# Kernel optimization log

Measured on AMD Instinct MI355X. Metric: run time of the kernel, lower is better.

## Reference

```python
import jax, jax.numpy as jnp
import numpy as np

V = 12288      # HEALPix vertices (nside=32)
C_IN = 128
C_OUT = 128
K = 4          # Chebyshev polynomial degree
DEG = 9        # nnz per Laplacian row (8 neighbors + self)
B = 8
BN_EPS = 1e-5


def setup_inputs() -> dict:
    key = jax.random.key(0)
    kx, kc, kv, kw = jax.random.split(key, 4)
    x = jax.random.normal(kx, (B, V, C_IN), dtype=jnp.float32)
    # sparse Laplacian as COO edge list: 9 entries per row
    lap_rows = jnp.repeat(jnp.arange(V, dtype=jnp.int32), DEG)          # [E]
    lap_cols = jax.random.randint(kc, (V * DEG,), 0, V, dtype=jnp.int32)
    lap_vals = jax.random.normal(kv, (V * DEG,), dtype=jnp.float32) * 0.1
    # Chebyshev weight [Fin*K, Fout] (Fin-major, K-minor, matching [B,V,Fin,K] reshape)
    weight = jax.random.normal(kw, (C_IN * K, C_OUT), dtype=jnp.float32) * (1.0 / np.sqrt(C_IN * K))
    gamma = jnp.ones((C_OUT,), dtype=jnp.float32)
    beta = jnp.zeros((C_OUT,), dtype=jnp.float32)
    return {"x": x, "lap_rows": lap_rows, "lap_cols": lap_cols,
            "lap_vals": lap_vals, "weight": weight, "gamma": gamma, "beta": beta}


def reference(x, lap_rows, lap_cols, lap_vals, weight, gamma, beta):
    b, v, c = x.shape
    k = weight.shape[0] // c

    def spmm(y):
        # y: [B, V, C] -> L @ y along vertex dim
        y2 = y.transpose(1, 0, 2).reshape(v, b * c)                 # [V, B*C]
        g = lap_vals[:, None] * y2[lap_cols]                        # [E, B*C]
        out = jnp.zeros((v, b * c), dtype=y.dtype).at[lap_rows].add(g)
        return out.reshape(v, b, c).transpose(1, 0, 2)              # [B, V, C]

    # Chebyshev recursion: T0 = x, T1 = L x, Tk = 2 L T_{k-1} - T_{k-2}
    terms = [x]
    if k > 1:
        terms.append(spmm(x))
    for _ in range(2, k):
        terms.append(2.0 * spmm(terms[-1]) - terms[-2])
    xk = jnp.stack(terms, axis=-1)                                  # [B, V, C, K]
    conv = jnp.einsum('bvck,cko->bvo', xk.reshape(b, v, c, k),
                      weight.reshape(c, k, -1))                     # [B, V, Cout]

    # BatchNorm1d over [B, Cout, V]: stats over (batch, vertices) per channel
    h = conv.transpose(0, 2, 1)                                     # [B, Cout, V]
    mean = jnp.mean(h, axis=(0, 2), keepdims=True)
    var = jnp.var(h, axis=(0, 2), keepdims=True)
    hn = (h - mean) * jax.lax.rsqrt(var + BN_EPS)
    return hn * gamma[None, :, None] + beta[None, :, None]          # [B, Cout, V]
```

## Files before the change

### kernel.cpp

```cpp
#include <hip/hip_runtime.h>

#define NV    12288
#define CIN   128
#define COUT  128
#define DEG   9
#define NB    8
#define NROWS (NB * NV)
#define KTOT  512
#define BM    384

typedef unsigned short bfu;
typedef __attribute__((ext_vector_type(8))) short short8;
typedef __attribute__((ext_vector_type(4))) float floatx4;
typedef __attribute__((ext_vector_type(4))) unsigned short ushort4v;

__device__ __forceinline__ float bf2f(unsigned short u) {
    union { unsigned int i; float f; } x;
    x.i = ((unsigned int)u) << 16;
    return x.f;
}
__device__ __forceinline__ unsigned short f2bf(float f) {
    union { float f; unsigned int i; } x;
    x.f = f;
    unsigned int r = x.i + 0x7FFFu + ((x.i >> 16) & 1u);
    return (unsigned short)(r >> 16);
}
__device__ __forceinline__ void gload16(const void* g, void* l) {
    __builtin_amdgcn_global_load_lds(
        (const __attribute__((address_space(1))) unsigned int*)g,
        (__attribute__((address_space(3))) unsigned int*)l, 16, 0, 0);
}

__global__ __launch_bounds__(256)
void prep_kernel(const float* __restrict__ x, bfu* __restrict__ xb,
                 const float* __restrict__ W, bfu* __restrict__ Wt,
                 float* __restrict__ stats)
{
    const int blk = blockIdx.x;
    const int t   = threadIdx.x;
    if (blk < 6144) {
        const size_t i = ((size_t)blk * 256 + t) * 8;
        const float4 a = *reinterpret_cast<const float4*>(x + i);
        const float4 b = *reinterpret_cast<const float4*>(x + i + 4);
        short8 r;
        r[0] = (short)f2bf(a.x); r[1] = (short)f2bf(a.y);
        r[2] = (short)f2bf(a.z); r[3] = (short)f2bf(a.w);
        r[4] = (short)f2bf(b.x); r[5] = (short)f2bf(b.y);
        r[6] = (short)f2bf(b.z); r[7] = (short)f2bf(b.w);
        *reinterpret_cast<short8*>(xb + i) = r;
    } else if (blk < 6400) {
        const int i = (blk - 6144) * 256 + t;
        const int o = i >> 9;
        const int kap = i & 511;
        const int s = kap >> 7;
        const int c = kap & 127;
        Wt[i] = f2bf(W[(size_t)(c * 4 + s) * COUT + o]);
    } else {
        stats[t] = 0.f;
    }
}

__global__ __launch_bounds__(256)
void spmm_bf16(const bfu* __restrict__ src, const bfu* __restrict__ sub,
               bfu* __restrict__ outp, const int* __restrict__ cols,
               const float* __restrict__ vals)
{
    const int t  = threadIdx.x;
    const int b  = blockIdx.x & 7;
    const int vt = blockIdx.x >> 3;
    const int v  = vt * 16 + (t >> 4);
    const int c0 = (t & 15) * 8;

    int   ec[DEG];
    float ev[DEG];
#pragma unroll
    for (int e = 0; e < DEG; ++e) {
        ec[e] = cols[v * DEG + e];
        ev[e] = vals[v * DEG + e];
    }

    float acc[8];
#pragma unroll
    for (int j = 0; j < 8; ++j) acc[j] = 0.f;

    const size_t bbase = (size_t)b * NV * CIN;
#pragma unroll
    for (int e = 0; e < DEG; ++e) {
        const short8 s = *reinterpret_cast<const short8*>(
            src + bbase + (size_t)ec[e] * CIN + c0);
#pragma unroll
        for (int j = 0; j < 8; ++j)
            acc[j] = fmaf(ev[e], bf2f((unsigned short)s[j]), acc[j]);
    }

    if (sub != nullptr) {
        const short8 s0 = *reinterpret_cast<const short8*>(
            sub + bbase + (size_t)v * CIN + c0);
#pragma unroll
        for (int j = 0; j < 8; ++j)
            acc[j] = 2.f * acc[j] - bf2f((unsigned short)s0[j]);
    }

    short8 r;
#pragma unroll
    for (int j = 0; j < 8; ++j) r[j] = (short)f2bf(acc[j]);
    *reinterpret_cast<short8*>(outp + bbase + (size_t)v * CIN + c0) = r;
}

__global__ __launch_bounds__(512)
void gemm_mfma(const bfu* __restrict__ A0, const bfu* __restrict__ A1,
               const bfu* __restrict__ A2, const bfu* __restrict__ A3,
               const bfu* __restrict__ Wt, bfu* __restrict__ convT,
               float* __restrict__ gstats)
{
    extern __shared__ char smem[];

    const int t    = threadIdx.x;
    const int lane = t & 63;
    const int wid  = t >> 6;
    const int wr   = wid >> 1;
    const int wc   = wid & 1;
    const int rbase = blockIdx.x * BM;

    floatx4 acc[6][4];
#pragma unroll
    for (int m = 0; m < 6; ++m)
#pragma unroll
        for (int n = 0; n < 4; ++n) acc[m][n] = (floatx4){0.f, 0.f, 0.f, 0.f};

    const bfu* segs[4] = {A0, A1, A2, A3};

#define STAGE(KT, BUF)                                                        \
    {                                                                         \
        const bfu* As_ = segs[(KT) >> 2];                                     \
        const int  cb_ = ((KT) & 3) * 32;                                     \
        _Pragma("unroll")                                                     \
        for (int p = 0; p < 3; ++p) {                                         \
            const int flat = p * 512 + t;                                     \
            const int rr   = flat >> 2;                                       \
            const int ck   = flat & 3;                                        \
            gload16(As_ + (size_t)(rbase + rr) * CIN + cb_                    \
                        + ((ck ^ ((rr >> 1) & 3)) << 3),                      \
                    smem + (BUF) * 24576 + flat * 16);                        \
        }                                                                     \
        {                                                                     \
            const int nn = t >> 2;                                            \
            const int ck = t & 3;                                             \
            gload16(Wt + (size_t)nn * KTOT + (KT) * 32                        \
                       + ((ck ^ ((nn >> 1) & 3)) << 3),                       \
                    smem + 73728 + (BUF) * 8192 + t * 16);                    \
        }                                                                     \
    }

    STAGE(0, 0);
    STAGE(1, 1);
    asm volatile("s_waitcnt vmcnt(4)\n\ts_barrier" ::: "memory");

    const int rsw   = ((lane & 15) >> 1) & 3;
    const int chunk = ((lane >> 4) ^ rsw) * 16;

#pragma unroll
    for (int kt = 0; kt < 16; ++kt) {
        if (kt + 2 < 16) STAGE(kt + 2, (kt + 2) % 3);

        const char* abase = smem + (kt % 3) * 24576;
        const char* bbase = smem + 73728 + (kt % 3) * 8192;
        short8 a[6], b[4];
#pragma unroll
        for (int m = 0; m < 6; ++m)
            a[m] = *reinterpret_cast<const short8*>(
                abase + (wr * 96 + m * 16 + (lane & 15)) * 64 + chunk);
#pragma unroll
        for (int n = 0; n < 4; ++n)
            b[n] = *reinterpret_cast<const short8*>(
                bbase + (wc * 64 + n * 16 + (lane & 15)) * 64 + chunk);
#pragma unroll
        for (int m = 0; m < 6; ++m)
#pragma unroll
            for (int n = 0; n < 4; ++n)
                acc[m][n] = __builtin_amdgcn_mfma_f32_16x16x32_bf16(
                    a[m], b[n], acc[m][n], 0, 0, 0);

        if (kt <= 13)
            asm volatile("s_waitcnt vmcnt(4)\n\ts_barrier" ::: "memory");
        else if (kt == 14)
            asm volatile("s_waitcnt vmcnt(0)\n\ts_barrier" ::: "memory");
    }
#undef STAGE

    __syncthreads();
    float* sred = (float*)smem;
    float* qred = sred + COUT;
    if (t < COUT) { sred[t] = 0.f; qred[t] = 0.f; }
    __syncthreads();

    const int batch = rbase / NV;
    const int v0 = (rbase % NV) + wr * 96 + (lane >> 4) * 4;
    const int ob = wc * 64 + (lane & 15);

#pragma unroll
    for (int n = 0; n < 4; ++n) {
        const int o = ob + n * 16;
        float s = 0.f, q = 0.f;
        bfu* cbase = convT + ((size_t)batch * COUT + o) * NV + v0;
#pragma unroll
        for (int m = 0; m < 6; ++m) {
            const floatx4 v4 = acc[m][n];
            ushort4v r;
#pragma unroll
            for (int j = 0; j < 4; ++j) {
                r[j] = f2bf(v4[j]);
                s += v4[j];
                q = fmaf(v4[j], v4[j], q);
            }
            *reinterpret_cast<ushort4v*>(cbase + m * 16) = r;
        }
        s += __shfl_xor(s, 16); s += __shfl_xor(s, 32);
        q += __shfl_xor(q, 16); q += __shfl_xor(q, 32);
        if ((lane >> 4) == 0) {
            atomicAdd(&sred[o], s);
            atomicAdd(&qred[o], q);
        }
    }
    __syncthreads();
    if (t < COUT) {
        atomicAdd(&gstats[t], sred[t]);
        atomicAdd(&gstats[COUT + t], qred[t]);
    }
}

__global__ __launch_bounds__(256)
void normalize_bn(const bfu* __restrict__ convT, const float* __restrict__ stats,
                  const float* __restrict__ gamma, const float* __restrict__ beta,
                  float* __restrict__ outp)
{
    const size_t i = ((size_t)blockIdx.x * 256 + threadIdx.x) * 8;
    const int ch = (int)((i / NV) & (COUT - 1));
    const float invN = 1.0f / (float)NROWS;
    const float mean = stats[ch] * invN;
    const float var  = stats[COUT + ch] * invN - mean * mean;
    const float rsig = rsqrtf(var + 1e-5f);
    const float sc   = rsig * gamma[ch];
    const float sh   = beta[ch] - mean * sc;

    const short8 s = *reinterpret_cast<const short8*>(convT + i);
    float4 r0, r1;
    r0.x = fmaf(bf2f((unsigned short)s[0]), sc, sh);
    r0.y = fmaf(bf2f((unsigned short)s[1]), sc, sh);
    r0.z = fmaf(bf2f((unsigned short)s[2]), sc, sh);
    r0.w = fmaf(bf2f((unsigned short)s[3]), sc, sh);
    r1.x = fmaf(bf2f((unsigned short)s[4]), sc, sh);
    r1.y = fmaf(bf2f((unsigned short)s[5]), sc, sh);
    r1.z = fmaf(bf2f((unsigned short)s[6]), sc, sh);
    r1.w = fmaf(bf2f((unsigned short)s[7]), sc, sh);
    *reinterpret_cast<float4*>(outp + i)     = r0;
    *reinterpret_cast<float4*>(outp + i + 4) = r1;
}

extern "C" void kernel_launch(void* const* d_in, const int* in_sizes, int n_in,
                              void* d_out, int out_size, void* d_ws, size_t ws_size,
                              hipStream_t stream)
{
    (void)in_sizes; (void)n_in; (void)out_size; (void)ws_size;

    const float* x     = (const float*)d_in[0];
    const int*   cols  = (const int*)  d_in[2];
    const float* vals  = (const float*)d_in[3];
    const float* W     = (const float*)d_in[4];
    const float* gamma = (const float*)d_in[5];
    const float* beta  = (const float*)d_in[6];
    float*       out   = (float*)d_out;

    const size_t bufE = (size_t)NB * NV * CIN;

    bfu* xb    = (bfu*)d_ws;
    bfu* t1    = xb + bufE;
    bfu* t2    = t1 + bufE;
    bfu* t3    = t2 + bufE;
    bfu* convT = t3 + bufE;
    bfu* Wt    = convT + bufE;
    float* stats = (float*)(Wt + 65536);

    const dim3 blk(256);
    const int spmm_grid = (NV / 16) * NB;

    prep_kernel <<<6401, blk, 0, stream>>>(x, xb, W, Wt, stats);

    spmm_bf16 <<<spmm_grid, blk, 0, stream>>>(xb, nullptr, t1, cols, vals);
    spmm_bf16 <<<spmm_grid, blk, 0, stream>>>(t1, xb,      t2, cols, vals);
    spmm_bf16 <<<spmm_grid, blk, 0, stream>>>(t2, t1,      t3, cols, vals);

    gemm_mfma <<<NROWS / BM, dim3(512), 98304, stream>>>(
        xb, t1, t2, t3, Wt, convT, stats);

    normalize_bn <<<NROWS * CIN / (256 * 8), blk, 0, stream>>>(
        convT, stats, gamma, beta, out);
}
```

Before: 117.4 us.

## Fuse batchnorm normalize into GEMM via grid-wide barrier, dropping convT round trip

```diff
diff --git a/kernel.cpp b/kernel.cpp
--- a/kernel.cpp
+++ b/kernel.cpp
@@ -12,7 +12,6 @@
 typedef unsigned short bfu;
 typedef __attribute__((ext_vector_type(8))) short short8;
 typedef __attribute__((ext_vector_type(4))) float floatx4;
-typedef __attribute__((ext_vector_type(4))) unsigned short ushort4v;
 
 __device__ __forceinline__ float bf2f(unsigned short u) {
     union { unsigned int i; float f; } x;
@@ -57,6 +56,7 @@
         Wt[i] = f2bf(W[(size_t)(c * 4 + s) * COUT + o]);
     } else {
         stats[t] = 0.f;
+        if (t == 0) stats[2 * COUT] = 0.f;
     }
 }
 
@@ -107,11 +107,12 @@
     *reinterpret_cast<short8*>(outp + bbase + (size_t)v * CIN + c0) = r;
 }
 
-__global__ __launch_bounds__(512)
+__global__ __launch_bounds__(512, 2)
 void gemm_mfma(const bfu* __restrict__ A0, const bfu* __restrict__ A1,
                const bfu* __restrict__ A2, const bfu* __restrict__ A3,
-               const bfu* __restrict__ Wt, bfu* __restrict__ convT,
-               float* __restrict__ gstats)
+               const bfu* __restrict__ Wt, float* __restrict__ gstats,
+               const float* __restrict__ gamma, const float* __restrict__ beta,
+               float* __restrict__ outp)
 {
     extern __shared__ char smem[];
 
@@ -202,18 +203,14 @@
     for (int n = 0; n < 4; ++n) {
         const int o = ob + n * 16;
         float s = 0.f, q = 0.f;
-        bfu* cbase = convT + ((size_t)batch * COUT + o) * NV + v0;
 #pragma unroll
         for (int m = 0; m < 6; ++m) {
             const floatx4 v4 = acc[m][n];
-            ushort4v r;
 #pragma unroll
             for (int j = 0; j < 4; ++j) {
-                r[j] = f2bf(v4[j]);
                 s += v4[j];
                 q = fmaf(v4[j], v4[j], q);
             }
-            *reinterpret_cast<ushort4v*>(cbase + m * 16) = r;
         }
         s += __shfl_xor(s, 16); s += __shfl_xor(s, 32);
         q += __shfl_xor(q, 16); q += __shfl_xor(q, 32);
@@ -227,34 +224,38 @@
         atomicAdd(&gstats[t], sred[t]);
         atomicAdd(&gstats[COUT + t], qred[t]);
     }
-}
-
-__global__ __launch_bounds__(256)
-void normalize_bn(const bfu* __restrict__ convT, const float* __restrict__ stats,
-                  const float* __restrict__ gamma, const float* __restrict__ beta,
-                  float* __restrict__ outp)
-{
-    const size_t i = ((size_t)blockIdx.x * 256 + threadIdx.x) * 8;
-    const int ch = (int)((i / NV) & (COUT - 1));
+    __syncthreads();
+
+    unsigned int* ctr = (unsigned int*)&gstats[2 * COUT];
+    if (t == 0) {
+        __threadfence();
+        atomicAdd(ctr, 1u);
+        while (__hip_atomic_load(ctr, __ATOMIC_RELAXED,
+                                 __HIP_MEMORY_SCOPE_AGENT) < gridDim.x) { }
+        __threadfence();
+    }
+    __syncthreads();
+
     const float invN = 1.0f / (float)NROWS;
-    const float mean = stats[ch] * invN;
-    const float var  = stats[COUT + ch] * invN - mean * mean;
-    const float rsig = rsqrtf(var + 1e-5f);
-    const float sc   = rsig * gamma[ch];
-    const float sh   = beta[ch] - mean * sc;
-
-    const short8 s = *reinterpret_cast<const short8*>(convT + i);
-    float4 r0, r1;
-    r0.x = fmaf(bf2f((unsigned short)s[0]), sc, sh);
-    r0.y = fmaf(bf2f((unsigned short)s[1]), sc, sh);
-    r0.z = fmaf(bf2f((unsigned short)s[2]), sc, sh);
-    r0.w = fmaf(bf2f((unsigned short)s[3]), sc, sh);
-    r1.x = fmaf(bf2f((unsigned short)s[4]), sc, sh);
-    r1.y = fmaf(bf2f((unsigned short)s[5]), sc, sh);
-    r1.z = fmaf(bf2f((unsigned short)s[6]), sc, sh);
-    r1.w = fmaf(bf2f((unsigned short)s[7]), sc, sh);
-    *reinterpret_cast<float4*>(outp + i)     = r0;
-    *reinterpret_cast<float4*>(outp + i + 4) = r1;
+#pragma unroll
+    for (int n = 0; n < 4; ++n) {
+        const int o = ob + n * 16;
+        const float mean = gstats[o] * invN;
+        const float var  = gstats[COUT + o] * invN - mean * mean;
+        const float sc   = rsqrtf(var + 1e-5f) * gamma[o];
+        const float sh   = beta[o] - mean * sc;
+        float* obase = outp + ((size_t)batch * COUT + o) * NV + v0;
+#pragma unroll
+        for (int m = 0; m < 6; ++m) {
+            const floatx4 v4 = acc[m][n];
+            float4 r;
+            r.x = fmaf(v4[0], sc, sh);
+            r.y = fmaf(v4[1], sc, sh);
+            r.z = fmaf(v4[2], sc, sh);
+            r.w = fmaf(v4[3], sc, sh);
+            *reinterpret_cast<float4*>(obase + m * 16) = r;
+        }
+    }
 }
 
 extern "C" void kernel_launch(void* const* d_in, const int* in_sizes, int n_in,
@@ -277,8 +278,7 @@
     bfu* t1    = xb + bufE;
     bfu* t2    = t1 + bufE;
     bfu* t3    = t2 + bufE;
-    bfu* convT = t3 + bufE;
-    bfu* Wt    = convT + bufE;
+    bfu* Wt    = t3 + bufE;
     float* stats = (float*)(Wt + 65536);
 
     const dim3 blk(256);
@@ -291,8 +291,5 @@
     spmm_bf16 <<<spmm_grid, blk, 0, stream>>>(t2, t1,      t3, cols, vals);
 
     gemm_mfma <<<NROWS / BM, dim3(512), 98304, stream>>>(
-        xb, t1, t2, t3, Wt, convT, stats);
-
-    normalize_bn <<<NROWS * CIN / (256 * 8), blk, 0, stream>>>(
-        convT, stats, gamma, beta, out);
-}
+        xb, t1, t2, t3, Wt, stats, gamma, beta, out);
+}
```

New measurement: 115.6 us. About the same (-1.5%).
